# Optimization experiments

Hardware: AMD Instinct MI355X
Metric: run time of the kernel (lower is better)

## Reference

```python
import jax, jax.numpy as jnp
import numpy as np

D_MODEL = 1024
N_HEADS = 16
D_HEAD = 64
D_MLP = 4096
EPS = 1e-5
IGNORE = -1e5
ATTN_SCALE = float(np.sqrt(D_HEAD))


def setup_inputs() -> dict:
    key = jax.random.key(0)
    ks = jax.random.split(key, 10)
    s = 0.02
    return {
        "x": jax.random.normal(ks[0], (2, 2048, D_MODEL), jnp.float32),
        "ln1_w": jnp.ones((D_MODEL,), jnp.float32),
        "ln1_b": jnp.zeros((D_MODEL,), jnp.float32),
        "W_Q": jax.random.normal(ks[1], (N_HEADS, D_MODEL, D_HEAD), jnp.float32) * s,
        "W_K": jax.random.normal(ks[2], (N_HEADS, D_MODEL, D_HEAD), jnp.float32) * s,
        "W_V": jax.random.normal(ks[3], (N_HEADS, D_MODEL, D_HEAD), jnp.float32) * s,
        "W_O": jax.random.normal(ks[4], (N_HEADS, D_HEAD, D_MODEL), jnp.float32) * s,
        "b_Q": jnp.zeros((N_HEADS, D_HEAD), jnp.float32),
        "b_K": jnp.zeros((N_HEADS, D_HEAD), jnp.float32),
        "b_V": jnp.zeros((N_HEADS, D_HEAD), jnp.float32),
        "b_O": jnp.zeros((D_MODEL,), jnp.float32),
        "ln2_w": jnp.ones((D_MODEL,), jnp.float32),
        "ln2_b": jnp.zeros((D_MODEL,), jnp.float32),
        "W_in": jax.random.normal(ks[5], (D_MODEL, D_MLP), jnp.float32) * s,
        "b_in": jnp.zeros((D_MLP,), jnp.float32),
        "W_out": jax.random.normal(ks[6], (D_MLP, D_MODEL), jnp.float32) * s,
        "b_out": jnp.zeros((D_MODEL,), jnp.float32),
    }


def layer_norm(x, w, b):
    x = x - x.mean(axis=-1, keepdims=True)
    scale = jnp.sqrt((x * x).mean(axis=-1, keepdims=True) + EPS)
    return (x / scale) * w + b


def attention(x, W_Q, W_K, W_V, W_O, b_Q, b_K, b_V, b_O):
    # x: [b, s, d_model]; W_{Q,K,V}: [h, d_model, d_head]
    q = jnp.einsum('bsm,hmd->bshd', x, W_Q) + b_Q
    k = jnp.einsum('bsm,hmd->bshd', x, W_K) + b_K
    v = jnp.einsum('bsm,hmd->bshd', x, W_V) + b_V
    scores = jnp.einsum('bqhd,bkhd->bhqk', q, k) / ATTN_SCALE
    s = x.shape[1]
    mask = jnp.tril(jnp.ones((s, s), bool))  # causal
    scores = jnp.where(mask, scores, IGNORE)
    attn = jax.nn.softmax(scores, axis=-1)
    z = jnp.einsum('bkhd,bhqk->bqhd', v, attn)
    return jnp.einsum('bqhd,hdm->bqm', z, W_O) + b_O


def mlp(x, W_in, b_in, W_out, b_out):
    pre = jnp.einsum('bsm,mf->bsf', x, W_in) + b_in
    post = jax.nn.gelu(pre, approximate=False)
    return jnp.einsum('bsf,fm->bsm', post, W_out) + b_out


def reference(x, ln1_w, ln1_b, W_Q, W_K, W_V, W_O, b_Q, b_K, b_V, b_O,
              ln2_w, ln2_b, W_in, b_in, W_out, b_out):
    resid = x + attention(layer_norm(x, ln1_w, ln1_b), W_Q, W_K, W_V, W_O,
                          b_Q, b_K, b_V, b_O)
    out = resid + mlp(layer_norm(resid, ln2_w, ln2_b), W_in, b_in, W_out, b_out)
    return out
```

## Files before the change

### kernel.cpp

```cpp
#include <hip/hip_runtime.h>

typedef __attribute__((ext_vector_type(4))) float f32x4;
typedef __attribute__((ext_vector_type(8))) __bf16 bf16x8;
typedef __attribute__((ext_vector_type(8))) unsigned short ushort8;
typedef __attribute__((ext_vector_type(4))) unsigned short ushort4v;

union UBF8 { ushort8 u; bf16x8 b; };
static __device__ __forceinline__ bf16x8 as_bf(ushort8 v) { UBF8 x; x.u = v; return x.b; }

static __device__ __forceinline__ unsigned short f2bf(float f) {
  union { float f; unsigned u; } v; v.f = f;
  unsigned r = v.u + 0x7fffu + ((v.u >> 16) & 1u);
  return (unsigned short)(r >> 16);
}

static __device__ __forceinline__ bf16x8 scale8(ushort8 u, float c) {
  ushort8 r;
#pragma unroll
  for (int j = 0; j < 8; j++) {
    union { unsigned u; float f; } t; t.u = ((unsigned)u[j]) << 16;
    r[j] = f2bf(t.f * c);
  }
  return as_bf(r);
}

static __device__ __forceinline__ float gelu_f(float x) {
  return 0.5f * x * (1.0f + erff(x * 0.70710678118654752f));
}

typedef const __attribute__((address_space(1))) void* gas_p;
typedef __attribute__((address_space(3))) void* las_p;
static __device__ __forceinline__ void gload16(const void* g, void* l) {
  __builtin_amdgcn_global_load_lds((gas_p)g, (las_p)l, 16, 0, 0);
}

__global__ __launch_bounds__(256) void ln_kernel(
    const float* __restrict__ in, const float* __restrict__ w,
    const float* __restrict__ b, unsigned short* __restrict__ out)
{
  const int row = blockIdx.x, t = threadIdx.x;
  const float4 v = *reinterpret_cast<const float4*>(in + (size_t)row * 1024 + t * 4);
  float s = v.x + v.y + v.z + v.w;
#pragma unroll
  for (int o = 32; o >= 1; o >>= 1) s += __shfl_xor(s, o);
  __shared__ float ps[4], qs[4];
  if ((t & 63) == 0) ps[t >> 6] = s;
  __syncthreads();
  const float mean = (ps[0] + ps[1] + ps[2] + ps[3]) * (1.0f / 1024.0f);
  const float cx = v.x - mean, cy = v.y - mean, cz = v.z - mean, cw = v.w - mean;
  float q = cx * cx + cy * cy + cz * cz + cw * cw;
#pragma unroll
  for (int o = 32; o >= 1; o >>= 1) q += __shfl_xor(q, o);
  if ((t & 63) == 0) qs[t >> 6] = q;
  __syncthreads();
  const float rstd = rsqrtf((qs[0] + qs[1] + qs[2] + qs[3]) * (1.0f / 1024.0f) + 1e-5f);
  const float4 wv = *reinterpret_cast<const float4*>(w + t * 4);
  const float4 bv = *reinterpret_cast<const float4*>(b + t * 4);
  ushort4v o4;
  o4.x = f2bf(cx * rstd * wv.x + bv.x);
  o4.y = f2bf(cy * rstd * wv.y + bv.y);
  o4.z = f2bf(cz * rstd * wv.z + bv.z);
  o4.w = f2bf(cw * rstd * wv.w + bv.w);
  *reinterpret_cast<ushort4v*>(out + (size_t)row * 1024 + t * 4) = o4;
}

__global__ __launch_bounds__(256) void conv_qkv_kernel(
    const float* __restrict__ WQ, const float* __restrict__ WK,
    const float* __restrict__ WV, unsigned short* __restrict__ out)
{
  __shared__ float t[32][33];
  const int mat_h = blockIdx.z;
  const int mat = mat_h >> 4, h = mat_h & 15;
  const float* W = (mat == 0 ? WQ : (mat == 1 ? WK : WV)) + (size_t)h * (1024 * 64);
  const int m0 = blockIdx.x * 32;
  const int d0 = blockIdx.y * 32;
  const int tx = threadIdx.x & 31, ty = threadIdx.x >> 5;
#pragma unroll
  for (int j = 0; j < 4; j++)
    t[ty + j * 8][tx] = W[(size_t)(m0 + ty + j * 8) * 64 + d0 + tx];
  __syncthreads();
  const size_t obase = (size_t)(mat * 1024 + h * 64 + d0);
#pragma unroll
  for (int j = 0; j < 4; j++)
    out[(obase + ty + j * 8) * 1024 + m0 + tx] = f2bf(t[tx][ty + j * 8]);
}

__global__ __launch_bounds__(256) void pack_bias_kernel(
    const float* __restrict__ bQ, const float* __restrict__ bK,
    const float* __restrict__ bV, float* __restrict__ out)
{
  const int i = blockIdx.x * 256 + threadIdx.x;
  if (i < 1024) out[i] = bQ[i];
  else if (i < 2048) out[i] = bK[i - 1024];
  else if (i < 3072) out[i] = bV[i - 2048];
}

__global__ __launch_bounds__(256) void transpose_cast_kernel(
    const float* __restrict__ in, unsigned short* __restrict__ out, int R, int C)
{
  __shared__ float t[32][33];
  const int c0 = blockIdx.x * 32, r0 = blockIdx.y * 32;
  const int tx = threadIdx.x & 31, ty = threadIdx.x >> 5;
#pragma unroll
  for (int j = 0; j < 4; j++)
    t[ty + j * 8][tx] = in[(size_t)(r0 + ty + j * 8) * C + c0 + tx];
  __syncthreads();
#pragma unroll
  for (int j = 0; j < 4; j++)
    out[(size_t)(c0 + ty + j * 8) * R + r0 + tx] = f2bf(t[tx][ty + j * 8]);
}

template <int BN, int EPI>
__global__ __launch_bounds__(256) void gemm_kernel(
    const unsigned short* __restrict__ A, const unsigned short* __restrict__ Bt,
    void* Cout, const float* __restrict__ bias, const float* resid,
    int N, int K, int gx)
{
  constexpr int BM = 128, BK = 64;
  constexpr int NF = (BN == 128) ? 4 : 2;
  __shared__ __align__(16) unsigned short As[BM * BK];
  __shared__ __align__(16) unsigned short Bs[BN * BK];
  const int tid = threadIdx.x, lane = tid & 63, w = tid >> 6;
  const int nwg = gridDim.x;
  int id = blockIdx.x;
  id = (id & 7) * (nwg >> 3) + (id >> 3);
  const int bm = (id % gx) * BM, bn = (id / gx) * BN;

  const int l15 = lane & 15, hi = lane >> 4;
  const int wr = w >> 1, wc = w & 1;
  const int arow = wr * 64;
  const int brow = (BN == 128) ? wc * 64 : wc * 32;
  f32x4 acc[4][NF] = {};

  const int srow = lane >> 3;
  const int scol = ((lane & 7) ^ srow) * 8;
  const unsigned short* Ag[BM / 32];
  const unsigned short* Bg[BN / 32];
#pragma unroll
  for (int it = 0; it < BM / 32; it++)
    Ag[it] = A + (size_t)(bm + 8 * (it * 4 + w) + srow) * K + scol;
#pragma unroll
  for (int it = 0; it < BN / 32; it++)
    Bg[it] = Bt + (size_t)(bn + 8 * (it * 4 + w) + srow) * K + scol;

  const char* Asb = (const char*)As;
  const char* Bsb = (const char*)Bs;
  const int rsw = (l15 & 7) << 4;

  for (int k0 = 0; k0 < K; k0 += BK) {
    __syncthreads();
#pragma unroll
    for (int it = 0; it < BM / 32; it++)
      gload16(Ag[it] + k0, &As[(it * 4 + w) * 8 * BK]);
#pragma unroll
    for (int it = 0; it < BN / 32; it++)
      gload16(Bg[it] + k0, &Bs[(it * 4 + w) * 8 * BK]);
    __syncthreads();

    bf16x8 af[2][4], bfr[2][NF];
#pragma unroll
    for (int kk = 0; kk < 2; kk++) {
      const int cb = kk * 64 + hi * 16;
#pragma unroll
      for (int mf = 0; mf < 4; mf++) {
        const int R = arow + mf * 16 + l15;
        af[kk][mf] = as_bf(*reinterpret_cast<const ushort8*>(Asb + R * (BK * 2) + (cb ^ rsw)));
      }
#pragma unroll
      for (int nf = 0; nf < NF; nf++) {
        const int R = brow + nf * 16 + l15;
        bfr[kk][nf] = as_bf(*reinterpret_cast<const ushort8*>(Bsb + R * (BK * 2) + (cb ^ rsw)));
      }
    }
#pragma unroll
    for (int kk = 0; kk < 2; kk++)
#pragma unroll
      for (int mf = 0; mf < 4; mf++)
#pragma unroll
        for (int nf = 0; nf < NF; nf++)
          acc[mf][nf] = __builtin_amdgcn_mfma_f32_16x16x32_bf16(af[kk][mf], bfr[kk][nf], acc[mf][nf], 0, 0, 0);
  }

  const int row0 = bm + arow + 4 * hi;
  const int col0 = bn + brow + l15;
#pragma unroll
  for (int mf = 0; mf < 4; mf++) {
#pragma unroll
    for (int nf = 0; nf < NF; nf++) {
#pragma unroll
      for (int i = 0; i < 4; i++) {
        const int row = row0 + mf * 16 + i;
        const int col = col0 + nf * 16;
        float v = acc[mf][nf][i] + bias[col];
        if (EPI == 1) v += resid[(size_t)row * N + col];
        if (EPI == 2) v = gelu_f(v);
        if (EPI == 1) ((float*)Cout)[(size_t)row * N + col] = v;
        else          ((unsigned short*)Cout)[(size_t)row * N + col] = f2bf(v);
      }
    }
  }
}

__global__ __launch_bounds__(256) void attn_kernel(
    const unsigned short* __restrict__ qkv, unsigned short* __restrict__ zout)
{
  __shared__ __align__(16) unsigned short Ks[64 * 72];
  __shared__ __align__(16) unsigned short Vt[64 * 72];
  __shared__ __align__(16) unsigned short Ps[4 * 16 * 72];
  const int tid = threadIdx.x, lane = tid & 63, w = tid >> 6;
  const int l15 = lane & 15, hi = lane >> 4, ko = hi * 8;
  const int j = blockIdx.x, bh = blockIdx.y;
  const int cA = j, cB = 31 - j;
  const size_t tok0 = (size_t)(bh >> 4) * 2048;
  const int h = bh & 15;
  const int qoff = h * 64, koff = 1024 + h * 64, voff = 2048 + h * 64;
  const int rowA = cA * 64 + w * 16;
  const int rowB = cB * 64 + w * 16;
  const float qscale = 0.125f * 1.44269504f;

  bf16x8 qfA[2], qfB[2];
#pragma unroll
  for (int kf = 0; kf < 2; kf++) {
    qfA[kf] = scale8(*reinterpret_cast<const ushort8*>(qkv + (tok0 + rowA + l15) * 3072 + qoff + kf * 32 + ko), qscale);
    qfB[kf] = scale8(*reinterpret_cast<const ushort8*>(qkv + (tok0 + rowB + l15) * 3072 + qoff + kf * 32 + ko), qscale);
  }

  float mA[4], lA[4], mB[4], lB[4];
  f32x4 zA[4], zB[4];
#pragma unroll
  for (int i = 0; i < 4; i++) {
    mA[i] = -1e30f; lA[i] = 0.0f; mB[i] = -1e30f; lB[i] = 0.0f;
#pragma unroll
    for (int nf = 0; nf < 4; nf++) { zA[nf][i] = 0.0f; zB[nf][i] = 0.0f; }
  }

  unsigned short* Pw = Ps + w * (16 * 72);
  const int sr = tid >> 3, scol = (tid & 7) * 8;

  for (int kt = 0; kt <= cB; kt++) {
    __syncthreads();
#pragma unroll
    for (int it = 0; it < 2; it++) {
      const int rr = sr + it * 32;
      const size_t gb = (tok0 + kt * 64 + rr) * 3072;
      *reinterpret_cast<ushort8*>(&Ks[rr * 72 + scol]) =
          *reinterpret_cast<const ushort8*>(qkv + gb + koff + scol);
      ushort8 vv = *reinterpret_cast<const ushort8*>(qkv + gb + voff + scol);
#pragma unroll
      for (int jj = 0; jj < 8; jj++) {
        const int d = scol + jj;
        Vt[d * 72 + (rr ^ (((d >> 3) & 7) << 3))] = vv[jj];
      }
    }
    __syncthreads();

    bf16x8 kb[4][2], vb[4][2];
#pragma unroll
    for (int nf = 0; nf < 4; nf++)
#pragma unroll
      for (int kf = 0; kf < 2; kf++) {
        kb[nf][kf] = as_bf(*reinterpret_cast<const ushort8*>(&Ks[(nf * 16 + l15) * 72 + kf * 32 + ko]));
        const int d = nf * 16 + l15;
        vb[nf][kf] = as_bf(*reinterpret_cast<const ushort8*>(
            &Vt[d * 72 + ((kf * 32 + ko) ^ (((d >> 3) & 7) << 3))]));
      }

    const bool actA = (kt <= cA);

    f32x4 sA[4] = {}, sB[4] = {};
    __builtin_amdgcn_s_setprio(1);
#pragma unroll
    for (int nf = 0; nf < 4; nf++)
#pragma unroll
      for (int kf = 0; kf < 2; kf++) {
        if (actA) sA[nf] = __builtin_amdgcn_mfma_f32_16x16x32_bf16(qfA[kf], kb[nf][kf], sA[nf], 0, 0, 0);
        sB[nf] = __builtin_amdgcn_mfma_f32_16x16x32_bf16(qfB[kf], kb[nf][kf], sB[nf], 0, 0, 0);
      }
    __builtin_amdgcn_s_setprio(0);

    auto process = [&](f32x4* s, float* mrow, float* lrow, f32x4* accz, int rowbase, bool dm) {
#pragma unroll
      for (int i = 0; i < 4; i++) {
        const int rg = rowbase + 4 * hi + i;
        float mx = -1e30f;
#pragma unroll
        for (int nf = 0; nf < 4; nf++) {
          float v = s[nf][i];
          if (dm && (kt * 64 + nf * 16 + l15 > rg)) v = -1e30f;
          s[nf][i] = v;
          mx = fmaxf(mx, v);
        }
#pragma unroll
        for (int o = 1; o <= 8; o <<= 1) mx = fmaxf(mx, __shfl_xor(mx, o));
        const float mnew = fmaxf(mrow[i], mx);
        const float fct = exp2f(mrow[i] - mnew);
        mrow[i] = mnew;
        float rs = 0.0f;
#pragma unroll
        for (int nf = 0; nf < 4; nf++) {
          const float pv = exp2f(s[nf][i] - mnew);
          s[nf][i] = pv;
          rs += pv;
        }
#pragma unroll
        for (int o = 1; o <= 8; o <<= 1) rs += __shfl_xor(rs, o);
        lrow[i] = lrow[i] * fct + rs;
#pragma unroll
        for (int nf = 0; nf < 4; nf++) accz[nf][i] *= fct;
      }
#pragma unroll
      for (int i = 0; i < 4; i++)
#pragma unroll
        for (int nf = 0; nf < 4; nf++)
          Pw[(4 * hi + i) * 72 + ((nf * 16 + l15) ^ (hi << 3))] = f2bf(s[nf][i]);
#pragma unroll
      for (int kf = 0; kf < 2; kf++) {
        const bf16x8 pa = as_bf(*reinterpret_cast<const ushort8*>(
            &Pw[l15 * 72 + ((kf * 32 + ko) ^ (((l15 >> 2) & 3) << 3))]));
        __builtin_amdgcn_s_setprio(1);
#pragma unroll
        for (int nf = 0; nf < 4; nf++)
          accz[nf] = __builtin_amdgcn_mfma_f32_16x16x32_bf16(pa, vb[nf][kf], accz[nf], 0, 0, 0);
        __builtin_amdgcn_s_setprio(0);
      }
    };

    if (actA) process(sA, mA, lA, zA, rowA, kt >= cA);
    process(sB, mB, lB, zB, rowB, kt >= cB);
  }

  auto wb = [&](float* lrow, f32x4* accz, int rowbase) {
#pragma unroll
    for (int i = 0; i < 4; i++) {
      const float inv = 1.0f / lrow[i];
      const int srow = rowbase + 4 * hi + i;
#pragma unroll
      for (int nf = 0; nf < 4; nf++)
        zout[(tok0 + srow) * 1024 + h * 64 + nf * 16 + l15] = f2bf(accz[nf][i] * inv);
    }
  };
  wb(lA, zA, rowA);
  wb(lB, zB, rowB);
}

extern "C" void kernel_launch(void* const* d_in, const int* in_sizes, int n_in,
                              void* d_out, int out_size, void* d_ws, size_t ws_size,
                              hipStream_t stream)
{
  const float* x    = (const float*)d_in[0];
  const float* ln1w = (const float*)d_in[1];
  const float* ln1b = (const float*)d_in[2];
  const float* WQ   = (const float*)d_in[3];
  const float* WK   = (const float*)d_in[4];
  const float* WV   = (const float*)d_in[5];
  const float* WO   = (const float*)d_in[6];
  const float* bQ   = (const float*)d_in[7];
  const float* bK   = (const float*)d_in[8];
  const float* bV   = (const float*)d_in[9];
  const float* bO   = (const float*)d_in[10];
  const float* ln2w = (const float*)d_in[11];
  const float* ln2b = (const float*)d_in[12];
  const float* Win  = (const float*)d_in[13];
  const float* bin  = (const float*)d_in[14];
  const float* Wout = (const float*)d_in[15];
  const float* bout = (const float*)d_in[16];
  float* out = (float*)d_out;

  char* ws = (char*)d_ws;
  unsigned short* bufA   = (unsigned short*)ws;
  unsigned short* bufB   = (unsigned short*)(ws + (size_t)(32 << 20));
  unsigned short* bufC   = (unsigned short*)(ws + (size_t)(40 << 20));
  float*          biasQKV = (float*)(ws + (size_t)(48 << 20));

  ln_kernel<<<4096, 256, 0, stream>>>(x, ln1w, ln1b, bufB);
  conv_qkv_kernel<<<dim3(32, 2, 48), 256, 0, stream>>>(WQ, WK, WV, bufC);
  pack_bias_kernel<<<12, 256, 0, stream>>>(bQ, bK, bV, biasQKV);
  gemm_kernel<128, 0><<<768, 256, 0, stream>>>(bufB, bufC, bufA, biasQKV, nullptr, 3072, 1024, 32);
  attn_kernel<<<dim3(16, 32), 256, 0, stream>>>(bufA, bufB);
  transpose_cast_kernel<<<dim3(32, 32), 256, 0, stream>>>(WO, bufC, 1024, 1024);
  gemm_kernel<64, 1><<<512, 256, 0, stream>>>(bufB, bufC, out, bO, x, 1024, 1024, 32);
  ln_kernel<<<4096, 256, 0, stream>>>(out, ln2w, ln2b, bufB);
  transpose_cast_kernel<<<dim3(128, 32), 256, 0, stream>>>(Win, bufC, 1024, 4096);
  gemm_kernel<128, 2><<<1024, 256, 0, stream>>>(bufB, bufC, bufA, bin, nullptr, 4096, 1024, 32);
  transpose_cast_kernel<<<dim3(32, 128), 256, 0, stream>>>(Wout, bufC, 4096, 1024);
  gemm_kernel<64, 1><<<512, 256, 0, stream>>>(bufA, bufC, out, bout, out, 1024, 4096, 32);
}
```

Baseline: 319.1 us.

## Compute softmax row sums via MFMA with ones, async-load K tile, use native bf16 convert

Replaces the per-row shuffle reduction of softmax probabilities with an extra MFMA against a vector of bf16 ones, so the row sum comes out of the matrix unit. K tiles now go to LDS through direct global-to-LDS loads with an XOR-swizzled unpadded layout instead of a register round-trip. The manual round-to-nearest bf16 conversion becomes a native cast. The row sum is now taken over bf16-rounded probabilities, which changes numerics slightly, and one extra MFMA is issued per k-fragment.

```diff
diff --git a/kernel.cpp b/kernel.cpp
--- a/kernel.cpp
+++ b/kernel.cpp
@@ -9,9 +9,7 @@
 static __device__ __forceinline__ bf16x8 as_bf(ushort8 v) { UBF8 x; x.u = v; return x.b; }
 
 static __device__ __forceinline__ unsigned short f2bf(float f) {
-  union { float f; unsigned u; } v; v.f = f;
-  unsigned r = v.u + 0x7fffu + ((v.u >> 16) & 1u);
-  return (unsigned short)(r >> 16);
+  union { __bf16 h; unsigned short u; } v; v.h = (__bf16)f; return v.u;
 }
 
 static __device__ __forceinline__ bf16x8 scale8(ushort8 u, float c) {
@@ -204,7 +202,7 @@
 __global__ __launch_bounds__(256) void attn_kernel(
     const unsigned short* __restrict__ qkv, unsigned short* __restrict__ zout)
 {
-  __shared__ __align__(16) unsigned short Ks[64 * 72];
+  __shared__ __align__(16) unsigned short Ks[64 * 64];
   __shared__ __align__(16) unsigned short Vt[64 * 72];
   __shared__ __align__(16) unsigned short Ps[4 * 16 * 72];
   const int tid = threadIdx.x, lane = tid & 63, w = tid >> 6;
@@ -225,6 +223,11 @@
     qfB[kf] = scale8(*reinterpret_cast<const ushort8*>(qkv + (tok0 + rowB + l15) * 3072 + qoff + kf * 32 + ko), qscale);
   }
 
+  UBF8 onesu;
+#pragma unroll
+  for (int jj = 0; jj < 8; jj++) onesu.u[jj] = 0x3F80;
+  const bf16x8 onesb = onesu.b;
+
   float mA[4], lA[4], mB[4], lB[4];
   f32x4 zA[4], zB[4];
 #pragma unroll
@@ -236,16 +239,23 @@
 
   unsigned short* Pw = Ps + w * (16 * 72);
   const int sr = tid >> 3, scol = (tid & 7) * 8;
+  const int srow8 = lane >> 3;
+  const int scol8 = ((lane & 7) ^ srow8) * 8;
+  const char* Ksb = (const char*)Ks;
+  const int rswk = (l15 & 7) << 4;
 
   for (int kt = 0; kt <= cB; kt++) {
     __syncthreads();
 #pragma unroll
+    for (int t = 0; t < 2; t++) {
+      const int rbase = (w * 2 + t) * 8;
+      gload16(qkv + (tok0 + kt * 64 + rbase + srow8) * 3072 + koff + scol8,
+              &Ks[rbase * 64]);
+    }
+#pragma unroll
     for (int it = 0; it < 2; it++) {
       const int rr = sr + it * 32;
-      const size_t gb = (tok0 + kt * 64 + rr) * 3072;
-      *reinterpret_cast<ushort8*>(&Ks[rr * 72 + scol]) =
-          *reinterpret_cast<const ushort8*>(qkv + gb + koff + scol);
-      ushort8 vv = *reinterpret_cast<const ushort8*>(qkv + gb + voff + scol);
+      ushort8 vv = *reinterpret_cast<const ushort8*>(qkv + (tok0 + kt * 64 + rr) * 3072 + voff + scol);
 #pragma unroll
       for (int jj = 0; jj < 8; jj++) {
         const int d = scol + jj;
@@ -259,7 +269,8 @@
     for (int nf = 0; nf < 4; nf++)
 #pragma unroll
       for (int kf = 0; kf < 2; kf++) {
-        kb[nf][kf] = as_bf(*reinterpret_cast<const ushort8*>(&Ks[(nf * 16 + l15) * 72 + kf * 32 + ko]));
+        const int R = nf * 16 + l15;
+        kb[nf][kf] = as_bf(*reinterpret_cast<const ushort8*>(Ksb + R * 128 + ((kf * 64 + hi * 16) ^ rswk)));
         const int d = nf * 16 + l15;
         vb[nf][kf] = as_bf(*reinterpret_cast<const ushort8*>(
             &Vt[d * 72 + ((kf * 32 + ko) ^ (((d >> 3) & 7) << 3))]));
@@ -279,6 +290,7 @@
     __builtin_amdgcn_s_setprio(0);
 
     auto process = [&](f32x4* s, float* mrow, float* lrow, f32x4* accz, int rowbase, bool dm) {
+      float fct[4];
 #pragma unroll
       for (int i = 0; i < 4; i++) {
         const int rg = rowbase + 4 * hi + i;
@@ -293,36 +305,28 @@
 #pragma unroll
         for (int o = 1; o <= 8; o <<= 1) mx = fmaxf(mx, __shfl_xor(mx, o));
         const float mnew = fmaxf(mrow[i], mx);
-        const float fct = exp2f(mrow[i] - mnew);
+        fct[i] = exp2f(mrow[i] - mnew);
         mrow[i] = mnew;
-        float rs = 0.0f;
-#pragma unroll
-        for (int nf = 0; nf < 4; nf++) {
-          const float pv = exp2f(s[nf][i] - mnew);
-          s[nf][i] = pv;
-          rs += pv;
-        }
-#pragma unroll
-        for (int o = 1; o <= 8; o <<= 1) rs += __shfl_xor(rs, o);
-        lrow[i] = lrow[i] * fct + rs;
-#pragma unroll
-        for (int nf = 0; nf < 4; nf++) accz[nf][i] *= fct;
-      }
-#pragma unroll
-      for (int i = 0; i < 4; i++)
 #pragma unroll
         for (int nf = 0; nf < 4; nf++)
-          Pw[(4 * hi + i) * 72 + ((nf * 16 + l15) ^ (hi << 3))] = f2bf(s[nf][i]);
+          Pw[(4 * hi + i) * 72 + ((nf * 16 + l15) ^ (hi << 3))] = f2bf(exp2f(s[nf][i] - mnew));
+#pragma unroll
+        for (int nf = 0; nf < 4; nf++) accz[nf][i] *= fct[i];
+      }
+      f32x4 rsum = {};
 #pragma unroll
       for (int kf = 0; kf < 2; kf++) {
         const bf16x8 pa = as_bf(*reinterpret_cast<const ushort8*>(
             &Pw[l15 * 72 + ((kf * 32 + ko) ^ (((l15 >> 2) & 3) << 3))]));
         __builtin_amdgcn_s_setprio(1);
+        rsum = __builtin_amdgcn_mfma_f32_16x16x32_bf16(pa, onesb, rsum, 0, 0, 0);
 #pragma unroll
         for (int nf = 0; nf < 4; nf++)
           accz[nf] = __builtin_amdgcn_mfma_f32_16x16x32_bf16(pa, vb[nf][kf], accz[nf], 0, 0, 0);
         __builtin_amdgcn_s_setprio(0);
       }
+#pragma unroll
+      for (int i = 0; i < 4; i++) lrow[i] = lrow[i] * fct[i] + rsum[i];
     };
 
     if (actA) process(sA, mA, lA, zA, rowA, kt >= cA);
```

After: 380.6 us. +19.3%, slower.

## Double-buffer GEMM shared-memory tiles and use native bf16 conversion

Applied to the files above, without the earlier changes.

The GEMM kernel gets two shared-memory buffers for A and B, so the global-to-LDS load of the next K tile is issued before the MFMAs on the current tile run. This removes one barrier per iteration and lets memory traffic overlap with compute, at the cost of twice the LDS footprint, which may lower occupancy. f2bf now uses the compiler's native __bf16 cast, which may map to a hardware conversion instruction. The old manual rounding is kept as f2bf_rn for scale8 and the attention paths. The attention kernel also gets a launch bound asking for 4 blocks per CU, which can limit registers.

```diff
diff --git a/kernel.cpp b/kernel.cpp
--- a/kernel.cpp
+++ b/kernel.cpp
@@ -9,6 +9,10 @@
 static __device__ __forceinline__ bf16x8 as_bf(ushort8 v) { UBF8 x; x.u = v; return x.b; }
 
 static __device__ __forceinline__ unsigned short f2bf(float f) {
+  union { __bf16 h; unsigned short u; } v; v.h = (__bf16)f; return v.u;
+}
+
+static __device__ __forceinline__ unsigned short f2bf_rn(float f) {
   union { float f; unsigned u; } v; v.f = f;
   unsigned r = v.u + 0x7fffu + ((v.u >> 16) & 1u);
   return (unsigned short)(r >> 16);
@@ -19,7 +23,7 @@
 #pragma unroll
   for (int j = 0; j < 8; j++) {
     union { unsigned u; float f; } t; t.u = ((unsigned)u[j]) << 16;
-    r[j] = f2bf(t.f * c);
+    r[j] = f2bf_rn(t.f * c);
   }
   return as_bf(r);
 }
@@ -118,8 +122,8 @@
 {
   constexpr int BM = 128, BK = 64;
   constexpr int NF = (BN == 128) ? 4 : 2;
-  __shared__ __align__(16) unsigned short As[BM * BK];
-  __shared__ __align__(16) unsigned short Bs[BN * BK];
+  __shared__ __align__(16) unsigned short As[2][BM * BK];
+  __shared__ __align__(16) unsigned short Bs[2][BN * BK];
   const int tid = threadIdx.x, lane = tid & 63, w = tid >> 6;
   const int nwg = gridDim.x;
   int id = blockIdx.x;
@@ -143,20 +147,27 @@
   for (int it = 0; it < BN / 32; it++)
     Bg[it] = Bt + (size_t)(bn + 8 * (it * 4 + w) + srow) * K + scol;
 
-  const char* Asb = (const char*)As;
-  const char* Bsb = (const char*)Bs;
   const int rsw = (l15 & 7) << 4;
-
-  for (int k0 = 0; k0 < K; k0 += BK) {
-    __syncthreads();
+  const int NT = K / BK;
+
+  auto stage = [&](int k0, int buf) {
 #pragma unroll
     for (int it = 0; it < BM / 32; it++)
-      gload16(Ag[it] + k0, &As[(it * 4 + w) * 8 * BK]);
+      gload16(Ag[it] + k0, &As[buf][(it * 4 + w) * 8 * BK]);
 #pragma unroll
     for (int it = 0; it < BN / 32; it++)
-      gload16(Bg[it] + k0, &Bs[(it * 4 + w) * 8 * BK]);
-    __syncthreads();
-
+      gload16(Bg[it] + k0, &Bs[buf][(it * 4 + w) * 8 * BK]);
+  };
+
+  stage(0, 0);
+  __syncthreads();
+  int cur = 0;
+
+  for (int t = 0; t < NT; ++t) {
+    if (t + 1 < NT) stage((t + 1) * BK, cur ^ 1);
+
+    const char* Asb = (const char*)As[cur];
+    const char* Bsb = (const char*)Bs[cur];
     bf16x8 af[2][4], bfr[2][NF];
 #pragma unroll
     for (int kk = 0; kk < 2; kk++) {
@@ -179,6 +190,9 @@
 #pragma unroll
         for (int nf = 0; nf < NF; nf++)
           acc[mf][nf] = __builtin_amdgcn_mfma_f32_16x16x32_bf16(af[kk][mf], bfr[kk][nf], acc[mf][nf], 0, 0, 0);
+
+    __syncthreads();
+    cur ^= 1;
   }
 
   const int row0 = bm + arow + 4 * hi;
@@ -201,7 +215,7 @@
   }
 }
 
-__global__ __launch_bounds__(256) void attn_kernel(
+__global__ __launch_bounds__(256, 4) void attn_kernel(
     const unsigned short* __restrict__ qkv, unsigned short* __restrict__ zout)
 {
   __shared__ __align__(16) unsigned short Ks[64 * 72];
@@ -312,7 +326,7 @@
       for (int i = 0; i < 4; i++)
 #pragma unroll
         for (int nf = 0; nf < 4; nf++)
-          Pw[(4 * hi + i) * 72 + ((nf * 16 + l15) ^ (hi << 3))] = f2bf(s[nf][i]);
+          Pw[(4 * hi + i) * 72 + ((nf * 16 + l15) ^ (hi << 3))] = f2bf_rn(s[nf][i]);
 #pragma unroll
       for (int kf = 0; kf < 2; kf++) {
         const bf16x8 pa = as_bf(*reinterpret_cast<const ushort8*>(
@@ -336,7 +350,7 @@
       const int srow = rowbase + 4 * hi + i;
 #pragma unroll
       for (int nf = 0; nf < 4; nf++)
-        zout[(tok0 + srow) * 1024 + h * 64 + nf * 16 + l15] = f2bf(accz[nf][i] * inv);
+        zout[(tok0 + srow) * 1024 + h * 64 + nf * 16 + l15] = f2bf_rn(accz[nf][i] * inv);
     }
   };
   wb(lA, zA, rowA);
```

Result: slower. 545.3 us (+70.9%).
